# Kernel tuning notes

Measured on AMD Instinct MI355X. Metric: run time of the kernel, lower is better.

## Reference

```python
import jax, jax.numpy as jnp
import numpy as np

EPS = 1e-5
NUM_GROUPS = 32


def setup_inputs() -> dict:
    key = jax.random.key(0)
    ks = jax.random.split(key, 4)
    b, c, h, w = 8, 512, 32, 32
    x = jax.random.normal(ks[0], (b, c, h, w), dtype=jnp.float32)
    gn_weight = jnp.ones((c,), dtype=jnp.float32)
    gn_bias = jnp.zeros((c,), dtype=jnp.float32)
    qkv_w = jax.random.normal(ks[1], (3 * c, c), dtype=jnp.float32) * (1.0 / np.sqrt(c))
    qkv_b = jnp.zeros((3 * c,), dtype=jnp.float32)
    proj_w = jax.random.normal(ks[2], (c, c), dtype=jnp.float32) * (1.0 / np.sqrt(c))
    proj_b = jnp.zeros((c,), dtype=jnp.float32)
    return {"x": x, "gn_weight": gn_weight, "gn_bias": gn_bias,
            "qkv_w": qkv_w, "qkv_b": qkv_b, "proj_w": proj_w, "proj_b": proj_b}


def _group_norm(x, weight, bias):
    b, c, h, w = x.shape
    xg = x.reshape(b, NUM_GROUPS, c // NUM_GROUPS, h, w)
    mean = xg.mean(axis=(2, 3, 4), keepdims=True)
    var = xg.var(axis=(2, 3, 4), keepdims=True)
    xn = ((xg - mean) * jax.lax.rsqrt(var + EPS)).reshape(b, c, h, w)
    return xn * weight[None, :, None, None] + bias[None, :, None, None]


def reference(x, gn_weight, gn_bias, qkv_w, qkv_b, proj_w, proj_b):
    b, c, h, w = x.shape
    scale = c ** (-0.5)
    xn = _group_norm(x, gn_weight, gn_bias)
    # 1x1 conv == per-pixel matmul over channels
    qkv = jnp.einsum('bchw,oc->bohw', xn, qkv_w) + qkv_b[None, :, None, None]
    q, k, v = jnp.split(qkv.reshape(b, 3 * c, h * w), 3, axis=1)  # each [b, c, N]
    attn = jax.nn.softmax(jnp.einsum('bci,bcj->bij', q, k) * scale, axis=-1)
    out = jnp.einsum('bij,bcj->bci', attn, v).reshape(b, c, h, w)
    proj = jnp.einsum('bchw,oc->bohw', out, proj_w) + proj_b[None, :, None, None]
    return x + proj
```

## Files before the change

### kernel.cpp

```cpp
#include <hip/hip_runtime.h>
#include <cmath>

constexpr int Bsz = 8, Cch = 512, NPIX = 1024;
constexpr int NG = 32, CPG = 16;

typedef __attribute__((ext_vector_type(4))) float f32x4;
typedef __attribute__((ext_vector_type(8))) short s16x8;

#define GLOBAL_AS __attribute__((address_space(1)))
#define LDS_AS __attribute__((address_space(3)))

__device__ inline short f2bf(float f) {
  union { float f; unsigned u; } c = {f};
  unsigned r = (c.u + 0x7fffu + ((c.u >> 16) & 1u)) >> 16;
  return (short)r;
}

__device__ inline float wave_reduce_sum(float v) {
#pragma unroll
  for (int off = 32; off > 0; off >>= 1) v += __shfl_xor(v, off, 64);
  return v;
}

__global__ __launch_bounds__(256) void prep_kernel(
    const float* __restrict__ x, const float* __restrict__ w,
    const float* __restrict__ bb, short* __restrict__ xnt,
    const float* __restrict__ in1, short* __restrict__ out1, int n1,
    const float* __restrict__ in2, short* __restrict__ out2, int n2,
    float* __restrict__ lsum) {
  __shared__ float sm[8];
  if (blockIdx.x == 1280) {
    float4 z = {0.f, 0.f, 0.f, 0.f};
    float4* p = (float4*)lsum;
#pragma unroll
    for (int i = 0; i < 8; ++i) p[threadIdx.x + i * 256] = z;
    return;
  }
  if (blockIdx.x >= 256) {
    const int i = ((blockIdx.x - 256) * 256 + threadIdx.x) * 4;
    const float* in = in1;
    short* out = out1;
    int j = i;
    if (i >= n1) { in = in2; out = out2; j = i - n1; }
    if (j + 3 < (i >= n1 ? n2 : n1)) {
      float4 v = *(const float4*)(in + j);
      short o[4] = {f2bf(v.x), f2bf(v.y), f2bf(v.z), f2bf(v.w)};
      *(uint2*)(out + j) = *(const uint2*)o;
    }
    return;
  }
  const int bg = ((int)blockIdx.x & 7) * 32 + ((int)blockIdx.x >> 3);
  const int b = bg >> 5, g = bg & 31;
  const float* xp = x + ((size_t)(b * Cch + g * CPG)) * NPIX;
  float s = 0.f, ss = 0.f;
  for (int i = threadIdx.x * 4; i < CPG * NPIX; i += 1024) {
    float4 v = *(const float4*)(xp + i);
    s += v.x + v.y + v.z + v.w;
    ss += v.x * v.x + v.y * v.y + v.z * v.z + v.w * v.w;
  }
  s = wave_reduce_sum(s);
  ss = wave_reduce_sum(ss);
  const int wv = threadIdx.x >> 6;
  if ((threadIdx.x & 63) == 0) { sm[wv] = s; sm[4 + wv] = ss; }
  __syncthreads();
  const float tsum = sm[0] + sm[1] + sm[2] + sm[3];
  const float tsq = sm[4] + sm[5] + sm[6] + sm[7];
  const float inv_n = 1.0f / (CPG * NPIX);
  const float mean = tsum * inv_n;
  const float rstd = rsqrtf(tsq * inv_n - mean * mean + 1e-5f);
  float wc[CPG], bc[CPG];
#pragma unroll
  for (int c = 0; c < CPG; ++c) {
    wc[c] = w[g * CPG + c] * rstd;
    bc[c] = bb[g * CPG + c] - mean * wc[c];
  }
  const int p0 = threadIdx.x * 4;
  short ov[4][CPG];
#pragma unroll
  for (int c = 0; c < CPG; ++c) {
    float4 v = *(const float4*)(xp + (size_t)c * NPIX + p0);
    ov[0][c] = f2bf(v.x * wc[c] + bc[c]);
    ov[1][c] = f2bf(v.y * wc[c] + bc[c]);
    ov[2][c] = f2bf(v.z * wc[c] + bc[c]);
    ov[3][c] = f2bf(v.w * wc[c] + bc[c]);
  }
#pragma unroll
  for (int j = 0; j < 4; ++j) {
    short* op = xnt + ((size_t)(b * NPIX + p0 + j)) * Cch + g * CPG;
    *(uint4*)op = *(const uint4*)&ov[j][0];
    *(uint4*)(op + 8) = *(const uint4*)&ov[j][8];
  }
}

template <int BN, int EPI>
__global__ __launch_bounds__(512, 2) void gemm256(
    const short* __restrict__ A, const short* __restrict__ B, int K, int lda,
    int ldb, long sA, long sB, const float* __restrict__ bias, float alpha,
    void* __restrict__ Cp, long sC, int ldc, void* __restrict__ C2p, long sC2) {
  constexpr int FN = BN / 64;
  constexpr int NBI = BN / 128;
  constexpr int G = 2 + NBI;
  constexpr int ASZ = 256 * 32;
  constexpr int BSZ = BN * 32;
  __shared__ __align__(16) short Asl[2 * ASZ];
  __shared__ __align__(16) short Bsl[2 * BSZ];
  const int t = threadIdx.x;
  const int lane = t & 63, wave = t >> 6;
  const int wm = wave >> 2, wn = wave & 3;

  const int gx = gridDim.x, gy = gridDim.y;
  const int nwg = gx * gy * (int)gridDim.z;
  int flat = (int)blockIdx.x + gx * ((int)blockIdx.y + gy * (int)blockIdx.z);
  flat = (flat & 7) * (nwg >> 3) + (flat >> 3);
  const int bx = flat % gx;
  const int rem = flat / gx;
  const int by = rem % gy;
  const int bz = rem / gy;

  const int m0 = by * 256, n0 = bx * BN;
  A += sA * bz;
  B += sB * bz;

  const short* ga[2];
  const short* gb[NBI];
  short* la[2];
  short* lb[NBI];
#pragma unroll
  for (int i = 0; i < 2; ++i) {
    const int c = i * 512 + t;
    const int row = ((c >> 6) << 4) + (c & 15);
    const int q = (c >> 4) & 3;
    ga[i] = A + (size_t)(m0 + row) * lda + q * 8;
    la[i] = Asl + c * 8;
  }
#pragma unroll
  for (int i = 0; i < NBI; ++i) {
    const int c = i * 512 + t;
    const int row = ((c >> 6) << 4) + (c & 15);
    const int q = (c >> 4) & 3;
    gb[i] = B + (size_t)(n0 + row) * ldb + q * 8;
    lb[i] = Bsl + c * 8;
  }

  auto stage = [&](int slot) {
#pragma unroll
    for (int i = 0; i < 2; ++i) {
      __builtin_amdgcn_global_load_lds((const GLOBAL_AS void*)ga[i],
                                       (LDS_AS void*)(la[i] + slot * ASZ), 16,
                                       0, 0);
      ga[i] += 32;
    }
#pragma unroll
    for (int i = 0; i < NBI; ++i) {
      __builtin_amdgcn_global_load_lds((const GLOBAL_AS void*)gb[i],
                                       (LDS_AS void*)(lb[i] + slot * BSZ), 16,
                                       0, 0);
      gb[i] += 32;
    }
  };

  f32x4 acc[8][FN] = {};
  const int NT = K >> 5;

  stage(0);
  for (int kt = 0; kt < NT; ++kt) {
    const int cur = kt & 1;
    if (kt + 1 < NT) {
      stage(cur ^ 1);
      asm volatile("s_waitcnt vmcnt(%0)\n\ts_barrier" ::"n"(G) : "memory");
    } else {
      asm volatile("s_waitcnt vmcnt(0)\n\ts_barrier" ::: "memory");
    }
    const short* Ab = Asl + cur * ASZ;
    const short* Bb = Bsl + cur * BSZ;
    s16x8 af[4], bf[FN];
#pragma unroll
    for (int j = 0; j < 4; ++j)
      af[j] = *(const s16x8*)(Ab + (wm * 8 + j) * 512 + lane * 8);
#pragma unroll
    for (int in = 0; in < FN; ++in)
      bf[in] = *(const s16x8*)(Bb + (wn * FN + in) * 512 + lane * 8);
    __builtin_amdgcn_s_setprio(1);
#pragma unroll
    for (int im = 0; im < 4; ++im)
#pragma unroll
      for (int in = 0; in < FN; ++in)
        acc[im][in] = __builtin_amdgcn_mfma_f32_16x16x32_bf16(
            af[im], bf[in], acc[im][in], 0, 0, 0);
    __builtin_amdgcn_s_setprio(0);
    asm volatile("s_waitcnt lgkmcnt(0)\n\ts_barrier" ::: "memory");
#pragma unroll
    for (int j = 0; j < 4; ++j)
      af[j] = *(const s16x8*)(Ab + (wm * 8 + 4 + j) * 512 + lane * 8);
    __builtin_amdgcn_s_setprio(1);
#pragma unroll
    for (int im = 0; im < 4; ++im)
#pragma unroll
      for (int in = 0; in < FN; ++in)
        acc[4 + im][in] = __builtin_amdgcn_mfma_f32_16x16x32_bf16(
            af[im], bf[in], acc[4 + im][in], 0, 0, 0);
    __builtin_amdgcn_s_setprio(0);
    asm volatile("s_waitcnt lgkmcnt(0)\n\ts_barrier" ::: "memory");
  }

  const int quad = lane >> 4, nn = lane & 15;
  if (EPI == 1) {
    short* Cs = (short*)Cp + sC * bz;
    float* L = (float*)C2p + sC2 * bz;
#pragma unroll
    for (int im = 0; im < 8; ++im) {
      const int m = m0 + wm * 128 + im * 16 + quad * 4;
      float rs[4] = {0.f, 0.f, 0.f, 0.f};
#pragma unroll
      for (int in = 0; in < FN; ++in) {
        const int n = n0 + wn * (FN * 16) + in * 16 + nn;
#pragma unroll
        for (int r = 0; r < 4; ++r) {
          const float e = __expf(acc[im][in][r] * alpha);
          rs[r] += e;
          Cs[(size_t)(m + r) * ldc + n] = f2bf(e);
        }
      }
#pragma unroll
      for (int off = 1; off < 16; off <<= 1)
#pragma unroll
        for (int r = 0; r < 4; ++r) rs[r] += __shfl_xor(rs[r], off, 64);
      if (nn == 0) {
#pragma unroll
        for (int r = 0; r < 4; ++r) atomicAdd(&L[m + r], rs[r]);
      }
    }
    return;
  }
#pragma unroll
  for (int im = 0; im < 8; ++im) {
#pragma unroll
    for (int in = 0; in < FN; ++in) {
      const int m = m0 + wm * 128 + im * 16 + quad * 4;
      const int n = n0 + wn * (FN * 16) + in * 16 + nn;
      if (m0 < 1024) {
        short* Cq = (short*)Cp + sC * bz;
        short o[4];
#pragma unroll
        for (int r = 0; r < 4; ++r) o[r] = f2bf(acc[im][in][r] + bias[m + r]);
        *(uint2*)(Cq + (size_t)n * ldc + m) = *(const uint2*)o;
      } else {
        short* Cv = (short*)C2p + sC2 * bz;
#pragma unroll
        for (int r = 0; r < 4; ++r)
          Cv[(size_t)(m - 1024 + r) * ldc + n] =
              f2bf(acc[im][in][r] + bias[m + r]);
      }
    }
  }
}

template <int BM, int BN, int EPI>
__global__ __launch_bounds__(256) void mfma_gemm(
    const short* __restrict__ A, const short* __restrict__ B, int K, int lda,
    int ldb, long sA, long sB, const float* __restrict__ bias, float alpha,
    void* __restrict__ Cp, long sC, int ldc,
    const float* __restrict__ resid, long sR) {
  constexpr int FM = BM / 32, FN = BN / 32;
  constexpr int NA = BM / 64, NB = BN / 64;
  __shared__ __align__(16) short Asl[BM * 32];
  __shared__ __align__(16) short Bsl[BN * 32];
  const int t = threadIdx.x;
  const int lane = t & 63, wave = t >> 6;

  const int gx = gridDim.x, gy = gridDim.y;
  const int nwg = gx * gy * (int)gridDim.z;
  int flat = (int)blockIdx.x + gx * ((int)blockIdx.y + gy * (int)blockIdx.z);
  flat = (flat & 7) * (nwg >> 3) + (flat >> 3);
  const int bx = flat % gx;
  const int rem = flat / gx;
  const int by = rem % gy;
  const int bz = rem / gy;

  const int m0 = by * BM, n0 = bx * BN;
  A += sA * bz;
  B += sB * bz;

  const short* ga[NA];
  const short* gb[NB];
  short* la[NA];
  short* lb[NB];
#pragma unroll
  for (int i = 0; i < NA; ++i) {
    const int s = i * 256 + t;
    const int row = ((s >> 6) * 16) + (s & 15);
    const int q = (s >> 4) & 3;
    ga[i] = A + (size_t)(m0 + row) * lda + q * 8;
    la[i] = Asl + s * 8;
  }
#pragma unroll
  for (int i = 0; i < NB; ++i) {
    const int s = i * 256 + t;
    const int row = ((s >> 6) * 16) + (s & 15);
    const int q = (s >> 4) & 3;
    gb[i] = B + (size_t)(n0 + row) * ldb + q * 8;
    lb[i] = Bsl + s * 8;
  }

  f32x4 acc[FM][FN] = {};
  const int wm = wave & 1, wn = wave >> 1;

  for (int k0 = 0; k0 < K; k0 += 32) {
#pragma unroll
    for (int i = 0; i < NA; ++i) {
      __builtin_amdgcn_global_load_lds((const GLOBAL_AS void*)ga[i],
                                       (LDS_AS void*)la[i], 16, 0, 0);
      ga[i] += 32;
    }
#pragma unroll
    for (int i = 0; i < NB; ++i) {
      __builtin_amdgcn_global_load_lds((const GLOBAL_AS void*)gb[i],
                                       (LDS_AS void*)lb[i], 16, 0, 0);
      gb[i] += 32;
    }
    __syncthreads();
    s16x8 af[FM], bf[FN];
#pragma unroll
    for (int i = 0; i < FM; ++i)
      af[i] = *(const s16x8*)(Asl + (wm * FM + i) * 512 + lane * 8);
#pragma unroll
    for (int i = 0; i < FN; ++i)
      bf[i] = *(const s16x8*)(Bsl + (wn * FN + i) * 512 + lane * 8);
#pragma unroll
    for (int im = 0; im < FM; ++im)
#pragma unroll
      for (int in = 0; in < FN; ++in)
        acc[im][in] = __builtin_amdgcn_mfma_f32_16x16x32_bf16(
            af[im], bf[in], acc[im][in], 0, 0, 0);
    __syncthreads();
  }

  const int quad = lane >> 4, nn = lane & 15;
#pragma unroll
  for (int im = 0; im < FM; ++im) {
    float invl[4];
    if (EPI == 2) {
      const float* L = resid + sR * bz;
      const int m = m0 + (wm * FM + im) * 16 + quad * 4;
#pragma unroll
      for (int r = 0; r < 4; ++r) invl[r] = 1.0f / L[m + r];
    }
#pragma unroll
    for (int in = 0; in < FN; ++in) {
      const int m = m0 + (wm * FM + im) * 16 + quad * 4;
      const int n = n0 + (wn * FN + in) * 16 + nn;
      if (EPI == 2) {
        short* Cs = (short*)Cp + sC * bz;
#pragma unroll
        for (int r = 0; r < 4; ++r)
          Cs[(size_t)(m + r) * ldc + n] = f2bf(acc[im][in][r] * invl[r]);
      } else {
        float* Cf = (float*)Cp + sC * bz;
        const float* R = resid + sR * bz;
#pragma unroll
        for (int r = 0; r < 4; ++r)
          Cf[(size_t)(m + r) * ldc + n] =
              acc[im][in][r] + bias[m + r] + R[(size_t)(m + r) * ldc + n];
      }
    }
  }
}

extern "C" void kernel_launch(void* const* d_in, const int* in_sizes, int n_in,
                              void* d_out, int out_size, void* d_ws,
                              size_t ws_size, hipStream_t stream) {
  const float* x = (const float*)d_in[0];
  const float* gnw = (const float*)d_in[1];
  const float* gnb = (const float*)d_in[2];
  const float* qkvw = (const float*)d_in[3];
  const float* qkvb = (const float*)d_in[4];
  const float* projw = (const float*)d_in[5];
  const float* projb = (const float*)d_in[6];
  float* out = (float*)d_out;

  char* ws = (char*)d_ws;
  short* xnt = (short*)ws;
  short* qkt = (short*)(ws + (8ull << 20));
  short* vbuf = (short*)(ws + (24ull << 20));
  short* Pbuf = (short*)(ws + (32ull << 20));
  short* Ot = (short*)(ws + (48ull << 20));
  short* wq = (short*)(ws + (56ull << 20));
  short* wp = (short*)(ws + (58ull << 20));
  float* lsum = (float*)(ws + (60ull << 20));

  prep_kernel<<<1281, 256, 0, stream>>>(x, gnw, gnb, xnt, qkvw, wq, 1536 * 512,
                                        projw, wp, 512 * 512, lsum);

  gemm256<256, 0><<<dim3(4, 6, Bsz), 512, 0, stream>>>(
      wq, xnt, 512, 512, 512, 0L, 1024L * 512, qkvb, 1.0f, qkt, 1024L * 1024,
      1024, vbuf, 512L * 1024);

  const float scale = 1.0f / sqrtf(512.0f);
  gemm256<128, 1><<<dim3(8, 4, Bsz), 512, 0, stream>>>(
      qkt, qkt + 512, 512, 1024, 1024, 1024L * 1024, 1024L * 1024, nullptr,
      scale, Pbuf, 1024L * 1024, 1024, lsum, 1024L);

  mfma_gemm<128, 64, 2><<<dim3(8, 8, Bsz), 256, 0, stream>>>(
      Pbuf, vbuf, 1024, 1024, 1024, 1024L * 1024, 512L * 1024, nullptr, 1.0f,
      Ot, 1024L * 512, 512, lsum, 1024L);

  mfma_gemm<64, 128, 3><<<dim3(8, 8, Bsz), 256, 0, stream>>>(
      wp, Ot, 512, 512, 512, 0L, 1024L * 512, projb, 1.0f, out, 512L * 1024,
      1024, x, 512L * 1024);
}
```

Before: 201.6 us.

## Move QK^T softmax GEMM to mfma_gemm, simplify prep and drop mid-loop barrier

The QK^T exp-epilogue GEMM moves from the 256-row double-buffered gemm256 kernel to the simpler 128x128 mfma_gemm tile, with more blocks and 256 threads each. gemm256 is fixed to BN=256, and one LDS barrier between its two MFMA halves is removed. The group-norm prep kernel now writes one pixel per thread iteration with scalar loads, and the block remapping is dropped. The intent is to fix occupancy and grid balance and to cut a sync. In exchange the QK step loses double buffering, and prep uses narrower loads.

```diff
diff --git a/kernel.cpp b/kernel.cpp
--- a/kernel.cpp
+++ b/kernel.cpp
@@ -49,8 +49,7 @@
     }
     return;
   }
-  const int bg = ((int)blockIdx.x & 7) * 32 + ((int)blockIdx.x >> 3);
-  const int b = bg >> 5, g = bg & 31;
+  const int bg = blockIdx.x, b = bg >> 5, g = bg & 31;
   const float* xp = x + ((size_t)(b * Cch + g * CPG)) * NPIX;
   float s = 0.f, ss = 0.f;
   for (int i = threadIdx.x * 4; i < CPG * NPIX; i += 1024) {
@@ -74,34 +73,26 @@
     wc[c] = w[g * CPG + c] * rstd;
     bc[c] = bb[g * CPG + c] - mean * wc[c];
   }
-  const int p0 = threadIdx.x * 4;
-  short ov[4][CPG];
-#pragma unroll
-  for (int c = 0; c < CPG; ++c) {
-    float4 v = *(const float4*)(xp + (size_t)c * NPIX + p0);
-    ov[0][c] = f2bf(v.x * wc[c] + bc[c]);
-    ov[1][c] = f2bf(v.y * wc[c] + bc[c]);
-    ov[2][c] = f2bf(v.z * wc[c] + bc[c]);
-    ov[3][c] = f2bf(v.w * wc[c] + bc[c]);
-  }
-#pragma unroll
-  for (int j = 0; j < 4; ++j) {
-    short* op = xnt + ((size_t)(b * NPIX + p0 + j)) * Cch + g * CPG;
-    *(uint4*)op = *(const uint4*)&ov[j][0];
-    *(uint4*)(op + 8) = *(const uint4*)&ov[j][8];
-  }
-}
-
-template <int BN, int EPI>
+  for (int p = threadIdx.x; p < NPIX; p += 256) {
+    short ov[CPG];
+#pragma unroll
+    for (int c = 0; c < CPG; ++c)
+      ov[c] = f2bf(xp[(size_t)c * NPIX + p] * wc[c] + bc[c]);
+    short* op = xnt + ((size_t)(b * NPIX + p)) * Cch + g * CPG;
+    *(uint4*)op = *(const uint4*)&ov[0];
+    *(uint4*)(op + 8) = *(const uint4*)&ov[8];
+  }
+}
+
 __global__ __launch_bounds__(512, 2) void gemm256(
     const short* __restrict__ A, const short* __restrict__ B, int K, int lda,
     int ldb, long sA, long sB, const float* __restrict__ bias, float alpha,
     void* __restrict__ Cp, long sC, int ldc, void* __restrict__ C2p, long sC2) {
+  constexpr int BN = 256;
   constexpr int FN = BN / 64;
   constexpr int NBI = BN / 128;
   constexpr int G = 2 + NBI;
-  constexpr int ASZ = 256 * 32;
-  constexpr int BSZ = BN * 32;
+  constexpr int ASZ = 256 * 32, BSZ = BN * 32;
   __shared__ __align__(16) short Asl[2 * ASZ];
   __shared__ __align__(16) short Bsl[2 * BSZ];
   const int t = threadIdx.x;
@@ -188,7 +179,6 @@
         acc[im][in] = __builtin_amdgcn_mfma_f32_16x16x32_bf16(
             af[im], bf[in], acc[im][in], 0, 0, 0);
     __builtin_amdgcn_s_setprio(0);
-    asm volatile("s_waitcnt lgkmcnt(0)\n\ts_barrier" ::: "memory");
 #pragma unroll
     for (int j = 0; j < 4; ++j)
       af[j] = *(const s16x8*)(Ab + (wm * 8 + 4 + j) * 512 + lane * 8);
@@ -204,34 +194,6 @@
   }
 
   const int quad = lane >> 4, nn = lane & 15;
-  if (EPI == 1) {
-    short* Cs = (short*)Cp + sC * bz;
-    float* L = (float*)C2p + sC2 * bz;
-#pragma unroll
-    for (int im = 0; im < 8; ++im) {
-      const int m = m0 + wm * 128 + im * 16 + quad * 4;
-      float rs[4] = {0.f, 0.f, 0.f, 0.f};
-#pragma unroll
-      for (int in = 0; in < FN; ++in) {
-        const int n = n0 + wn * (FN * 16) + in * 16 + nn;
-#pragma unroll
-        for (int r = 0; r < 4; ++r) {
-          const float e = __expf(acc[im][in][r] * alpha);
-          rs[r] += e;
-          Cs[(size_t)(m + r) * ldc + n] = f2bf(e);
-        }
-      }
-#pragma unroll
-      for (int off = 1; off < 16; off <<= 1)
-#pragma unroll
-        for (int r = 0; r < 4; ++r) rs[r] += __shfl_xor(rs[r], off, 64);
-      if (nn == 0) {
-#pragma unroll
-        for (int r = 0; r < 4; ++r) atomicAdd(&L[m + r], rs[r]);
-      }
-    }
-    return;
-  }
 #pragma unroll
   for (int im = 0; im < 8; ++im) {
 #pragma unroll
@@ -259,7 +221,7 @@
 __global__ __launch_bounds__(256) void mfma_gemm(
     const short* __restrict__ A, const short* __restrict__ B, int K, int lda,
     int ldb, long sA, long sB, const float* __restrict__ bias, float alpha,
-    void* __restrict__ Cp, long sC, int ldc,
+    void* __restrict__ Cp, long sC, int ldc, void* __restrict__ C2p, long sC2,
     const float* __restrict__ resid, long sR) {
   constexpr int FM = BM / 32, FN = BN / 32;
   constexpr int NA = BM / 64, NB = BN / 64;
@@ -336,6 +298,34 @@
   }
 
   const int quad = lane >> 4, nn = lane & 15;
+  if (EPI == 1) {
+    short* Cs = (short*)Cp + sC * bz;
+    float* L = (float*)C2p + sC2 * bz;
+#pragma unroll
+    for (int im = 0; im < FM; ++im) {
+      const int m = m0 + (wm * FM + im) * 16 + quad * 4;
+      float rs[4] = {0.f, 0.f, 0.f, 0.f};
+#pragma unroll
+      for (int in = 0; in < FN; ++in) {
+        const int n = n0 + (wn * FN + in) * 16 + nn;
+#pragma unroll
+        for (int r = 0; r < 4; ++r) {
+          const float e = __expf(acc[im][in][r] * alpha);
+          rs[r] += e;
+          Cs[(size_t)(m + r) * ldc + n] = f2bf(e);
+        }
+      }
+#pragma unroll
+      for (int off = 1; off < 16; off <<= 1)
+#pragma unroll
+        for (int r = 0; r < 4; ++r) rs[r] += __shfl_xor(rs[r], off, 64);
+      if (nn == 0) {
+#pragma unroll
+        for (int r = 0; r < 4; ++r) atomicAdd(&L[m + r], rs[r]);
+      }
+    }
+    return;
+  }
 #pragma unroll
   for (int im = 0; im < FM; ++im) {
     float invl[4];
@@ -391,20 +381,20 @@
   prep_kernel<<<1281, 256, 0, stream>>>(x, gnw, gnb, xnt, qkvw, wq, 1536 * 512,
                                         projw, wp, 512 * 512, lsum);
 
-  gemm256<256, 0><<<dim3(4, 6, Bsz), 512, 0, stream>>>(
+  gemm256<<<dim3(4, 6, Bsz), 512, 0, stream>>>(
       wq, xnt, 512, 512, 512, 0L, 1024L * 512, qkvb, 1.0f, qkt, 1024L * 1024,
       1024, vbuf, 512L * 1024);
 
   const float scale = 1.0f / sqrtf(512.0f);
-  gemm256<128, 1><<<dim3(8, 4, Bsz), 512, 0, stream>>>(
+  mfma_gemm<128, 128, 1><<<dim3(8, 8, Bsz), 256, 0, stream>>>(
       qkt, qkt + 512, 512, 1024, 1024, 1024L * 1024, 1024L * 1024, nullptr,
-      scale, Pbuf, 1024L * 1024, 1024, lsum, 1024L);
+      scale, Pbuf, 1024L * 1024, 1024, lsum, 1024L, nullptr, 0L);
 
   mfma_gemm<128, 64, 2><<<dim3(8, 8, Bsz), 256, 0, stream>>>(
       Pbuf, vbuf, 1024, 1024, 1024, 1024L * 1024, 512L * 1024, nullptr, 1.0f,
-      Ot, 1024L * 512, 512, lsum, 1024L);
+      Ot, 1024L * 512, 512, nullptr, 0L, lsum, 1024L);
 
   mfma_gemm<64, 128, 3><<<dim3(8, 8, Bsz), 256, 0, stream>>>(
       wp, Ot, 512, 512, 512, 0L, 1024L * 512, projb, 1.0f, out, 512L * 1024,
-      1024, x, 512L * 1024);
-}
+      1024, nullptr, 0L, x, 512L * 1024);
+}
```

Measured after the change: 199.0 us. Within noise of the previous version (-1.3%).
